# Performance work log

Hardware: AMD Instinct MI355X
Metric: run time of the kernel (lower is better)

Reference implementation:

```python
import jax, jax.numpy as jnp
import numpy as np

DIM = 512
HEADS = 8
DIM_HEAD = 64
CROSS_DIM = 768
FF_INNER = 4 * DIM  # 2048
SCALE = DIM_HEAD ** -0.5
EPS = 1e-5


def _layer_norm(x, g, b):
    mu = jnp.mean(x, axis=-1, keepdims=True)
    var = jnp.var(x, axis=-1, keepdims=True)
    return (x - mu) * jax.lax.rsqrt(var + EPS) * g + b


def _mha(q, k, v):
    # q: [B,Sq,D], k/v: [B,Sk,D] -> [B,Sq,D]
    B, Sq, D = q.shape
    Sk = k.shape[1]
    qh = q.reshape(B, Sq, HEADS, DIM_HEAD).transpose(0, 2, 1, 3)
    kh = k.reshape(B, Sk, HEADS, DIM_HEAD).transpose(0, 2, 1, 3)
    vh = v.reshape(B, Sk, HEADS, DIM_HEAD).transpose(0, 2, 1, 3)
    scores = jnp.einsum('bhqd,bhkd->bhqk', qh, kh) * SCALE
    probs = jax.nn.softmax(scores, axis=-1)
    out = jnp.einsum('bhqk,bhkd->bhqd', probs, vh)
    return out.transpose(0, 2, 1, 3).reshape(B, Sq, D)


def setup_inputs() -> dict:
    key = jax.random.key(0)
    ks = jax.random.split(key, 20)
    s = 0.02
    inp = {
        'x': jax.random.normal(ks[0], (8, 1024, DIM), jnp.float32),
        'enc': jax.random.normal(ks[1], (8, 77, CROSS_DIM), jnp.float32),
        # self-attention (attn1)
        'ln1_g': jnp.ones((DIM,), jnp.float32),
        'ln1_b': jnp.zeros((DIM,), jnp.float32),
        'wq1': jax.random.normal(ks[2], (DIM, DIM), jnp.float32) * s,
        'wk1': jax.random.normal(ks[3], (DIM, DIM), jnp.float32) * s,
        'wv1': jax.random.normal(ks[4], (DIM, DIM), jnp.float32) * s,
        'wo1': jax.random.normal(ks[5], (DIM, DIM), jnp.float32) * s,
        'bo1': jnp.zeros((DIM,), jnp.float32),
        # cross-attention (attn2)
        'ln2_g': jnp.ones((DIM,), jnp.float32),
        'ln2_b': jnp.zeros((DIM,), jnp.float32),
        'wq2': jax.random.normal(ks[6], (DIM, DIM), jnp.float32) * s,
        'wk2': jax.random.normal(ks[7], (CROSS_DIM, DIM), jnp.float32) * s,
        'wv2': jax.random.normal(ks[8], (CROSS_DIM, DIM), jnp.float32) * s,
        'wo2': jax.random.normal(ks[9], (DIM, DIM), jnp.float32) * s,
        'bo2': jnp.zeros((DIM,), jnp.float32),
        # feed-forward (GEGLU)
        'ln3_g': jnp.ones((DIM,), jnp.float32),
        'ln3_b': jnp.zeros((DIM,), jnp.float32),
        'wg': jax.random.normal(ks[10], (DIM, 2 * FF_INNER), jnp.float32) * s,
        'bg': jnp.zeros((2 * FF_INNER,), jnp.float32),
        'wf': jax.random.normal(ks[11], (FF_INNER, DIM), jnp.float32) * s,
        'bf': jnp.zeros((DIM,), jnp.float32),
    }
    return inp


def reference(x, enc, ln1_g, ln1_b, wq1, wk1, wv1, wo1, bo1,
              ln2_g, ln2_b, wq2, wk2, wv2, wo2, bo2,
              ln3_g, ln3_b, wg, bg, wf, bf):
    # self-attention block (pre-norm)
    h = _layer_norm(x, ln1_g, ln1_b)
    a = _mha(h @ wq1, h @ wk1, h @ wv1)
    x = x + a @ wo1 + bo1
    # cross-attention block (pre-norm)
    h = _layer_norm(x, ln2_g, ln2_b)
    a = _mha(h @ wq2, enc @ wk2, enc @ wv2)
    x = x + a @ wo2 + bo2
    # GEGLU feed-forward (pre-norm)
    h = _layer_norm(x, ln3_g, ln3_b)
    proj = h @ wg + bg
    u, g = jnp.split(proj, 2, axis=-1)
    ff = (u * jax.nn.gelu(g, approximate=False)) @ wf + bf
    return x + ff
```

## Files before the change

kernel.cpp:

```cpp
#include <hip/hip_runtime.h>


typedef _Float16 half8 __attribute__((ext_vector_type(8)));
typedef float f32x4 __attribute__((ext_vector_type(4)));

__device__ __forceinline__ f32x4 mfma16(half8 a, half8 b, f32x4 c) {
  return __builtin_amdgcn_mfma_f32_16x16x32_f16(a, b, c, 0, 0, 0);
}

__device__ __forceinline__ void gload16(const _Float16* g, _Float16* l) {
  __builtin_amdgcn_global_load_lds(
      (const __attribute__((address_space(1))) void*)g,
      (__attribute__((address_space(3))) void*)l, 16, 0, 0);
}

__global__ __launch_bounds__(256)
void transpose_cvt(const float* __restrict__ src, _Float16* __restrict__ dst,
                   int K, int N) {
  __shared__ float tile[32][33];
  const int tx = threadIdx.x, ty = threadIdx.y;
  const int n0 = blockIdx.x * 32, k0 = blockIdx.y * 32;
  #pragma unroll
  for (int j = ty; j < 32; j += 8)
    tile[j][tx] = src[(size_t)(k0 + j) * N + n0 + tx];
  __syncthreads();
  #pragma unroll
  for (int j = ty; j < 32; j += 8)
    dst[(size_t)(n0 + j) * K + k0 + tx] = (_Float16)tile[tx][j];
}

__global__ void cvt_f32_f16(const float* __restrict__ src,
                            _Float16* __restrict__ dst, int n) {
  int i = blockIdx.x * 256 + threadIdx.x;
  if (i < n) dst[i] = (_Float16)src[i];
}

__global__ __launch_bounds__(256)
void vt_kernel(const _Float16* __restrict__ src, _Float16* __restrict__ dst,
               int S, int srcStride, int dstStride) {
  __shared__ _Float16 tile[32][33];
  const int tx = threadIdx.x, ty = threadIdx.y;
  const int s0 = blockIdx.x * 32, d0 = blockIdx.y * 32, bh = blockIdx.z;
  const int b = bh >> 3, h = bh & 7;
  const _Float16* sp = src + (size_t)b * S * srcStride + h * 64 + d0;
  #pragma unroll
  for (int j = ty; j < 32; j += 8) {
    int s = s0 + j; if (s >= S) s = S - 1;
    tile[j][tx] = sp[(size_t)s * srcStride + tx];
  }
  __syncthreads();
  _Float16* dp = dst + ((size_t)bh * 64 + d0) * dstStride + s0;
  #pragma unroll
  for (int j = ty; j < 32; j += 8)
    dp[(size_t)j * dstStride + tx] = tile[tx][j];
}

__global__ __launch_bounds__(256)
void ln_kernel(const float* __restrict__ x, const float* __restrict__ g,
               const float* __restrict__ b, _Float16* __restrict__ out) {
  const int row = blockIdx.x, t = threadIdx.x;
  const float* xr = x + (size_t)row * 512;
  float v0 = xr[t], v1 = xr[t + 256];
  float s1 = v0 + v1, s2 = v0 * v0 + v1 * v1;
  #pragma unroll
  for (int m = 32; m >= 1; m >>= 1) {
    s1 += __shfl_xor(s1, m);
    s2 += __shfl_xor(s2, m);
  }
  __shared__ float red[8];
  if ((t & 63) == 0) { red[t >> 6] = s1; red[4 + (t >> 6)] = s2; }
  __syncthreads();
  s1 = red[0] + red[1] + red[2] + red[3];
  s2 = red[4] + red[5] + red[6] + red[7];
  const float mu = s1 * (1.0f / 512.0f);
  const float var = s2 * (1.0f / 512.0f) - mu * mu;
  const float rs = rsqrtf(var + 1e-5f);
  out[(size_t)row * 512 + t] = (_Float16)((v0 - mu) * rs * g[t] + b[t]);
  out[(size_t)row * 512 + t + 256] =
      (_Float16)((v1 - mu) * rs * g[t + 256] + b[t + 256]);
}

template <int EPI, int GWM, int GWN, int WM, int WN, int MW>
__global__ __launch_bounds__(256, MW)
void gemm_bt(const _Float16* __restrict__ A, const _Float16* __restrict__ BT,
             int M, int N, int K, int lda, int ldc,
             _Float16* Ch, float* Cf,
             const float* __restrict__ bias, const float* resid) {
  constexpr int BM = GWM * WM * 16;
  constexpr int BN = GWN * WN * 16;
  __shared__ __align__(16) _Float16 As[2][4 * BM * 8];
  __shared__ __align__(16) _Float16 Bs[2][4 * BN * 8];
  __shared__ __align__(16) _Float16 Bs2[(EPI == 2) ? 2 : 1]
                                      [(EPI == 2) ? 4 * BN * 8 : 8];

  const int t = threadIdx.x;
  const int m0 = blockIdx.y * BM, n0 = blockIdx.x * BN;
  const int lane = t & 63, wv = t >> 6;
  const int quad = lane >> 4, l15 = lane & 15;
  const int wm = wv / GWN, wn = wv % GWN;

  f32x4 zero4 = {0.f, 0.f, 0.f, 0.f};
  f32x4 acc[WM][WN];
  f32x4 acc2[(EPI == 2) ? WM : 1][(EPI == 2) ? WN : 1];
  #pragma unroll
  for (int mi = 0; mi < WM; mi++)
    #pragma unroll
    for (int ni = 0; ni < WN; ni++) acc[mi][ni] = zero4;
  if constexpr (EPI == 2) {
    #pragma unroll
    for (int mi = 0; mi < WM; mi++)
      #pragma unroll
      for (int ni = 0; ni < WN; ni++) acc2[mi][ni] = zero4;
  }

  auto stageAll = [&](int k0, int pb) {
    #pragma unroll
    for (int c = wv; c < BM / 16; c += 4) {
      const int s = c * 64 + lane;
      const int q = s / BM;
      const int r = s % BM;
      int rg = m0 + r; if (rg >= M) rg = M - 1;
      gload16(A + (size_t)rg * lda + k0 + q * 8, &As[pb][c * 512]);
    }
    #pragma unroll
    for (int c = wv; c < BN / 16; c += 4) {
      const int s = c * 64 + lane;
      const int q = s / BN;
      const int r = s % BN;
      gload16(BT + (size_t)(n0 + r) * K + k0 + q * 8, &Bs[pb][c * 512]);
      if constexpr (EPI == 2)
        gload16(BT + (size_t)(2048 + n0 + r) * K + k0 + q * 8,
                &Bs2[pb][c * 512]);
    }
  };

  stageAll(0, 0);
  __syncthreads();

  const int NIT = K >> 5;
  for (int it = 0; it < NIT; ++it) {
    const int cur = it & 1;
    if (it + 1 < NIT) stageAll((it + 1) << 5, cur ^ 1);

    half8 fa[WM], fb[WN], fb2[(EPI == 2) ? WN : 1];
    #pragma unroll
    for (int mi = 0; mi < WM; mi++)
      fa[mi] = *(const half8*)(&As[cur]
          [((size_t)quad * BM + wm * WM * 16 + mi * 16 + l15) * 8]);
    #pragma unroll
    for (int ni = 0; ni < WN; ni++) {
      fb[ni] = *(const half8*)(&Bs[cur]
          [((size_t)quad * BN + wn * WN * 16 + ni * 16 + l15) * 8]);
      if constexpr (EPI == 2)
        fb2[ni] = *(const half8*)(&Bs2[cur]
            [((size_t)quad * BN + wn * WN * 16 + ni * 16 + l15) * 8]);
    }
    #pragma unroll
    for (int mi = 0; mi < WM; mi++)
      #pragma unroll
      for (int ni = 0; ni < WN; ni++) {
        acc[mi][ni] = mfma16(fa[mi], fb[ni], acc[mi][ni]);
        if constexpr (EPI == 2)
          acc2[mi][ni] = mfma16(fa[mi], fb2[ni], acc2[mi][ni]);
      }
    __syncthreads();
  }

  #pragma unroll
  for (int mi = 0; mi < WM; mi++) {
    const int rbase = m0 + wm * WM * 16 + mi * 16 + quad * 4;
    #pragma unroll
    for (int r = 0; r < 4; r++) {
      const int row = rbase + r;
      if (row >= M) continue;
      #pragma unroll
      for (int ni = 0; ni < WN; ni++) {
        const int col = n0 + wn * WN * 16 + ni * 16 + l15;
        const float v = acc[mi][ni][r];
        if constexpr (EPI == 0) {
          Ch[(size_t)row * ldc + col] = (_Float16)v;
        } else if constexpr (EPI == 1) {
          Cf[(size_t)row * ldc + col] =
              resid[(size_t)row * ldc + col] + v + bias[col];
        } else {
          const float u = v + bias[col];
          const float gg = acc2[mi][ni][r] + bias[col + 2048];
          const float ge = 0.5f * gg * (1.0f + erff(gg * 0.70710678118f));
          Ch[(size_t)row * ldc + col] = (_Float16)(u * ge);
        }
      }
    }
  }
}

__global__ __launch_bounds__(256)
void attn2(const _Float16* __restrict__ Q, const _Float16* __restrict__ K,
           const _Float16* __restrict__ VT, _Float16* __restrict__ O,
           int qStride, int kStride, long kBatchStride,
           int vtStride, int Sk) {
  __shared__ __align__(16) _Float16 KsL[2][2048];
  __shared__ __align__(16) _Float16 VTsL[2][2048];
  __shared__ __align__(16) _Float16 Ps[4][2][16][40];

  const int t = threadIdx.x;
  const int w = t >> 6, lane = t & 63, quad = lane >> 4, l15 = lane & 15;
  const int bh = blockIdx.y, b = bh >> 3, h = bh & 7;
  const int q0 = blockIdx.x * 128 + w * 32;

  const _Float16 qscale = (_Float16)(0.125f * 1.44269504f);
  half8 qf[2][2];
  #pragma unroll
  for (int mi = 0; mi < 2; mi++)
    #pragma unroll
    for (int c = 0; c < 2; c++) {
      const _Float16* qp = Q +
          (size_t)(b * 1024 + q0 + mi * 16 + l15) * qStride +
          h * 64 + c * 32 + quad * 8;
      half8 v = *(const half8*)qp;
      #pragma unroll
      for (int j = 0; j < 8; j++) v[j] *= qscale;
      qf[mi][c] = v;
    }

  f32x4 zero4 = {0.f, 0.f, 0.f, 0.f};
  f32x4 oa[2][4];
  float psum[2][4];
  #pragma unroll
  for (int mi = 0; mi < 2; mi++) {
    #pragma unroll
    for (int nt = 0; nt < 4; nt++) oa[mi][nt] = zero4;
    #pragma unroll
    for (int r = 0; r < 4; r++) psum[mi][r] = 0.f;
  }

  const _Float16* kp = K + (size_t)b * kBatchStride + h * 64;
  const _Float16* vtp = VT + (size_t)bh * 64 * vtStride;
  const int ksk = t & 31, kc = t >> 7, kqd = (t >> 5) & 3;
  const int vd = t & 63, vqd = t >> 6;

  auto stageKV = [&](int skb, int pb) {
    int skc = skb + ksk; if (skc >= Sk) skc = Sk - 1;
    gload16(kp + (size_t)skc * kStride + kc * 32 + kqd * 8, &KsL[pb][t * 8]);
    gload16(vtp + (size_t)vd * vtStride + skb + vqd * 8, &VTsL[pb][t * 8]);
  };

  stageKV(0, 0);
  __syncthreads();

  int it = 0;
  for (int skb = 0; skb < Sk; skb += 32, ++it) {
    const int cur = it & 1;
    if (skb + 32 < Sk) stageKV(skb + 32, cur ^ 1);

    const bool tail = (skb + 32 > Sk);
    #pragma unroll
    for (int mi = 0; mi < 2; mi++) {
      #pragma unroll
      for (int ct = 0; ct < 2; ct++) {
        f32x4 s = zero4;
        half8 kb0 = *(const half8*)(&KsL[cur][(quad * 32 + ct * 16 + l15) * 8]);
        half8 kb1 =
            *(const half8*)(&KsL[cur][(128 + quad * 32 + ct * 16 + l15) * 8]);
        s = mfma16(qf[mi][0], kb0, s);
        s = mfma16(qf[mi][1], kb1, s);
        if (tail) {
          const bool valid = (skb + ct * 16 + l15) < Sk;
          #pragma unroll
          for (int r = 0; r < 4; r++)
            if (!valid) s[r] = -__builtin_inff();
        }
        #pragma unroll
        for (int r = 0; r < 4; r++) {
          const float e = exp2f(s[r]);
          psum[mi][r] += e;
          Ps[w][mi][quad * 4 + r][ct * 16 + l15] = (_Float16)e;
        }
      }
    }
    #pragma unroll
    for (int mi = 0; mi < 2; mi++) {
      const half8 pf = *(const half8*)(&Ps[w][mi][l15][quad * 8]);
      #pragma unroll
      for (int nt = 0; nt < 4; nt++) {
        const half8 vf =
            *(const half8*)(&VTsL[cur][(quad * 64 + nt * 16 + l15) * 8]);
        oa[mi][nt] = mfma16(pf, vf, oa[mi][nt]);
      }
    }
    __syncthreads();
  }

  #pragma unroll
  for (int mi = 0; mi < 2; mi++)
    #pragma unroll
    for (int r = 0; r < 4; r++) {
      #pragma unroll
      for (int mm = 1; mm < 16; mm <<= 1)
        psum[mi][r] += __shfl_xor(psum[mi][r], mm);
      psum[mi][r] = 1.0f / psum[mi][r];
    }

  #pragma unroll
  for (int mi = 0; mi < 2; mi++)
    #pragma unroll
    for (int nt = 0; nt < 4; nt++)
      #pragma unroll
      for (int r = 0; r < 4; r++) {
        const size_t row = (size_t)(b * 1024 + q0 + mi * 16 + quad * 4 + r);
        O[row * 512 + h * 64 + nt * 16 + l15] =
            (_Float16)(oa[mi][nt][r] * psum[mi][r]);
      }
}

extern "C" void kernel_launch(void* const* d_in, const int* in_sizes, int n_in,
                              void* d_out, int out_size, void* d_ws,
                              size_t ws_size, hipStream_t stream) {
  const float* x    = (const float*)d_in[0];
  const float* enc  = (const float*)d_in[1];
  const float* ln1g = (const float*)d_in[2];
  const float* ln1b = (const float*)d_in[3];
  const float* wq1  = (const float*)d_in[4];
  const float* wk1  = (const float*)d_in[5];
  const float* wv1  = (const float*)d_in[6];
  const float* wo1  = (const float*)d_in[7];
  const float* bo1  = (const float*)d_in[8];
  const float* ln2g = (const float*)d_in[9];
  const float* ln2b = (const float*)d_in[10];
  const float* wq2  = (const float*)d_in[11];
  const float* wk2  = (const float*)d_in[12];
  const float* wv2  = (const float*)d_in[13];
  const float* wo2  = (const float*)d_in[14];
  const float* bo2  = (const float*)d_in[15];
  const float* ln3g = (const float*)d_in[16];
  const float* ln3b = (const float*)d_in[17];
  const float* wg   = (const float*)d_in[18];
  const float* bg   = (const float*)d_in[19];
  const float* wf   = (const float*)d_in[20];
  const float* bfp  = (const float*)d_in[21];
  float* out = (float*)d_out;

  char* ws = (char*)d_ws;
  _Float16* qkvT  = (_Float16*)(ws + 0);
  _Float16* q2T   = (_Float16*)(ws + 1572864);
  _Float16* kv2T  = (_Float16*)(ws + 2097152);
  _Float16* wo1T  = (_Float16*)(ws + 3670016);
  _Float16* wo2T  = (_Float16*)(ws + 4194304);
  _Float16* wgT   = (_Float16*)(ws + 4718592);
  _Float16* wfT   = (_Float16*)(ws + 8912896);
  _Float16* hbuf  = (_Float16*)(ws + 11010048);
  _Float16* qkv   = (_Float16*)(ws + 19398656);
  _Float16* q2b   = (_Float16*)(ws + 44564480);
  _Float16* kv2b  = (_Float16*)(ws + 52953088);
  _Float16* attnb = (_Float16*)(ws + 54214656);
  _Float16* ench  = (_Float16*)(ws + 62603264);
  _Float16* ffb   = (_Float16*)(ws + 19398656);
  _Float16* VTself = hbuf;
  _Float16* VTc    = ench;

  const dim3 tb(32, 8);
  transpose_cvt<<<dim3(16, 16), tb, 0, stream>>>(wq1, qkvT, 512, 512);
  transpose_cvt<<<dim3(16, 16), tb, 0, stream>>>(wk1, qkvT + 512 * 512, 512, 512);
  transpose_cvt<<<dim3(16, 16), tb, 0, stream>>>(wv1, qkvT + 1024 * 512, 512, 512);
  transpose_cvt<<<dim3(16, 16), tb, 0, stream>>>(wo1, wo1T, 512, 512);
  transpose_cvt<<<dim3(16, 16), tb, 0, stream>>>(wq2, q2T, 512, 512);
  transpose_cvt<<<dim3(16, 24), tb, 0, stream>>>(wk2, kv2T, 768, 512);
  transpose_cvt<<<dim3(16, 24), tb, 0, stream>>>(wv2, kv2T + 512 * 768, 768, 512);
  transpose_cvt<<<dim3(16, 16), tb, 0, stream>>>(wo2, wo2T, 512, 512);
  transpose_cvt<<<dim3(128, 16), tb, 0, stream>>>(wg, wgT, 512, 4096);
  transpose_cvt<<<dim3(16, 64), tb, 0, stream>>>(wf, wfT, 2048, 512);
  cvt_f32_f16<<<(473088 + 255) / 256, 256, 0, stream>>>(enc, ench, 473088);

  ln_kernel<<<8192, 256, 0, stream>>>(x, ln1g, ln1b, hbuf);
  gemm_bt<0, 2, 2, 4, 4, 2><<<dim3(12, 64), 256, 0, stream>>>(
      hbuf, qkvT, 8192, 1536, 512, 512, 1536, qkv, nullptr, nullptr, nullptr);
  vt_kernel<<<dim3(32, 2, 64), tb, 0, stream>>>(qkv + 1024, VTself, 1024, 1536, 1024);
  attn2<<<dim3(8, 64), 256, 0, stream>>>(qkv, qkv + 512, VTself, attnb,
                                         1536, 1536, (long)1024 * 1536,
                                         1024, 1024);
  gemm_bt<1, 1, 4, 4, 2, 3><<<dim3(4, 128), 256, 0, stream>>>(
      attnb, wo1T, 8192, 512, 512, 512, 512, nullptr, out, bo1, x);

  ln_kernel<<<8192, 256, 0, stream>>>(out, ln2g, ln2b, hbuf);
  gemm_bt<0, 1, 4, 4, 2, 3><<<dim3(4, 128), 256, 0, stream>>>(
      hbuf, q2T, 8192, 512, 512, 512, 512, q2b, nullptr, nullptr, nullptr);
  gemm_bt<0, 1, 4, 4, 2, 3><<<dim3(8, 10), 256, 0, stream>>>(
      ench, kv2T, 616, 1024, 768, 768, 1024, kv2b, nullptr, nullptr, nullptr);
  vt_kernel<<<dim3(3, 2, 64), tb, 0, stream>>>(kv2b + 512, VTc, 77, 1024, 96);
  attn2<<<dim3(8, 64), 256, 0, stream>>>(q2b, kv2b, VTc, attnb,
                                         512, 1024, (long)77 * 1024, 96, 77);
  gemm_bt<1, 1, 4, 4, 2, 3><<<dim3(4, 128), 256, 0, stream>>>(
      attnb, wo2T, 8192, 512, 512, 512, 512, nullptr, out, bo2, out);

  ln_kernel<<<8192, 256, 0, stream>>>(out, ln3g, ln3b, hbuf);
  gemm_bt<2, 2, 2, 4, 2, 2><<<dim3(32, 64), 256, 0, stream>>>(
      hbuf, wgT, 8192, 2048, 512, 512, 2048, ffb, nullptr, bg, nullptr);
  gemm_bt<1, 1, 4, 4, 2, 3><<<dim3(4, 128), 256, 0, stream>>>(
      ffb, wfT, 8192, 512, 2048, 2048, 512, nullptr, out, bfp, out);
}
```

Measured before the change: 495.0 us.

## Merge weight prep launches and add XCD-aware block swizzle to GEMMs

```diff
diff --git a/kernel.cpp b/kernel.cpp
--- a/kernel.cpp
+++ b/kernel.cpp
@@ -14,12 +14,36 @@
       (__attribute__((address_space(3))) void*)l, 16, 0, 0);
 }
 
+struct PrepArgs {
+  const float* src[10];
+  _Float16* dst[10];
+  int K[10], N[10], base[10];
+  const float* enc;
+  _Float16* ench;
+  int encBase, nEnc;
+};
+
 __global__ __launch_bounds__(256)
-void transpose_cvt(const float* __restrict__ src, _Float16* __restrict__ dst,
-                   int K, int N) {
+void prep_all(PrepArgs pa) {
   __shared__ float tile[32][33];
+  const int bid = blockIdx.x;
   const int tx = threadIdx.x, ty = threadIdx.y;
-  const int n0 = blockIdx.x * 32, k0 = blockIdx.y * 32;
+  if (bid >= pa.encBase) {
+    const int i = (bid - pa.encBase) * 256 + ty * 32 + tx;
+    if (i < pa.nEnc) pa.ench[i] = (_Float16)pa.enc[i];
+    return;
+  }
+  int mi = 0;
+  #pragma unroll
+  for (int j = 1; j < 10; j++)
+    if (bid >= pa.base[j]) mi = j;
+  const int K = pa.K[mi], N = pa.N[mi];
+  const int rel = bid - pa.base[mi];
+  const int ntiles = N >> 5;
+  const int bx = rel % ntiles, by = rel / ntiles;
+  const float* src = pa.src[mi];
+  _Float16* dst = pa.dst[mi];
+  const int n0 = bx * 32, k0 = by * 32;
   #pragma unroll
   for (int j = ty; j < 32; j += 8)
     tile[j][tx] = src[(size_t)(k0 + j) * N + n0 + tx];
@@ -27,12 +51,6 @@
   #pragma unroll
   for (int j = ty; j < 32; j += 8)
     dst[(size_t)(n0 + j) * K + k0 + tx] = (_Float16)tile[tx][j];
-}
-
-__global__ void cvt_f32_f16(const float* __restrict__ src,
-                            _Float16* __restrict__ dst, int n) {
-  int i = blockIdx.x * 256 + threadIdx.x;
-  if (i < n) dst[i] = (_Float16)src[i];
 }
 
 __global__ __launch_bounds__(256)
@@ -80,7 +98,7 @@
       (_Float16)((v1 - mu) * rs * g[t + 256] + b[t + 256]);
 }
 
-template <int EPI, int GWM, int GWN, int WM, int WN, int MW>
+template <int EPI, int GWM, int GWN, int WM, int WN, int MW, int SWZ>
 __global__ __launch_bounds__(256, MW)
 void gemm_bt(const _Float16* __restrict__ A, const _Float16* __restrict__ BT,
              int M, int N, int K, int lda, int ldc,
@@ -94,7 +112,19 @@
                                       [(EPI == 2) ? 4 * BN * 8 : 8];
 
   const int t = threadIdx.x;
-  const int m0 = blockIdx.y * BM, n0 = blockIdx.x * BN;
+  const int NNB = (N + BN - 1) / BN;
+  int bm, bn;
+  if constexpr (SWZ) {
+    const int MG = (M / BM) >> 3;
+    const int xcd = blockIdx.x & 7;
+    const int s = blockIdx.x >> 3;
+    bm = xcd * MG + s % MG;
+    bn = s / MG;
+  } else {
+    bn = blockIdx.x % NNB;
+    bm = blockIdx.x / NNB;
+  }
+  const int m0 = bm * BM, n0 = bn * BN;
   const int lane = t & 63, wv = t >> 6;
   const int quad = lane >> 4, l15 = lane & 15;
   const int wm = wv / GWN, wn = wv % GWN;
@@ -357,43 +387,48 @@
   _Float16* VTself = hbuf;
   _Float16* VTc    = ench;
 
+  PrepArgs pa;
+  const float* srcs[10] = {wq1, wk1, wv1, wo1, wq2, wk2, wv2, wo2, wg, wf};
+  _Float16* dsts[10] = {qkvT, qkvT + 512 * 512, qkvT + 1024 * 512, wo1T, q2T,
+                        kv2T, kv2T + 512 * 768, wo2T, wgT, wfT};
+  const int Ks[10] = {512, 512, 512, 512, 512, 768, 768, 512, 512, 2048};
+  const int Ns[10] = {512, 512, 512, 512, 512, 512, 512, 512, 4096, 512};
+  int base = 0;
+  for (int i = 0; i < 10; i++) {
+    pa.src[i] = srcs[i]; pa.dst[i] = dsts[i];
+    pa.K[i] = Ks[i]; pa.N[i] = Ns[i]; pa.base[i] = base;
+    base += (Ks[i] >> 5) * (Ns[i] >> 5);
+  }
+  pa.enc = enc; pa.ench = ench; pa.encBase = base; pa.nEnc = 473088;
+  const int prepBlocks = base + (473088 + 255) / 256;
+  prep_all<<<prepBlocks, dim3(32, 8), 0, stream>>>(pa);
+
   const dim3 tb(32, 8);
-  transpose_cvt<<<dim3(16, 16), tb, 0, stream>>>(wq1, qkvT, 512, 512);
-  transpose_cvt<<<dim3(16, 16), tb, 0, stream>>>(wk1, qkvT + 512 * 512, 512, 512);
-  transpose_cvt<<<dim3(16, 16), tb, 0, stream>>>(wv1, qkvT + 1024 * 512, 512, 512);
-  transpose_cvt<<<dim3(16, 16), tb, 0, stream>>>(wo1, wo1T, 512, 512);
-  transpose_cvt<<<dim3(16, 16), tb, 0, stream>>>(wq2, q2T, 512, 512);
-  transpose_cvt<<<dim3(16, 24), tb, 0, stream>>>(wk2, kv2T, 768, 512);
-  transpose_cvt<<<dim3(16, 24), tb, 0, stream>>>(wv2, kv2T + 512 * 768, 768, 512);
-  transpose_cvt<<<dim3(16, 16), tb, 0, stream>>>(wo2, wo2T, 512, 512);
-  transpose_cvt<<<dim3(128, 16), tb, 0, stream>>>(wg, wgT, 512, 4096);
-  transpose_cvt<<<dim3(16, 64), tb, 0, stream>>>(wf, wfT, 2048, 512);
-  cvt_f32_f16<<<(473088 + 255) / 256, 256, 0, stream>>>(enc, ench, 473088);
 
   ln_kernel<<<8192, 256, 0, stream>>>(x, ln1g, ln1b, hbuf);
-  gemm_bt<0, 2, 2, 4, 4, 2><<<dim3(12, 64), 256, 0, stream>>>(
+  gemm_bt<0, 2, 2, 4, 4, 2, 1><<<768, 256, 0, stream>>>(
       hbuf, qkvT, 8192, 1536, 512, 512, 1536, qkv, nullptr, nullptr, nullptr);
   vt_kernel<<<dim3(32, 2, 64), tb, 0, stream>>>(qkv + 1024, VTself, 1024, 1536, 1024);
   attn2<<<dim3(8, 64), 256, 0, stream>>>(qkv, qkv + 512, VTself, attnb,
                                          1536, 1536, (long)1024 * 1536,
                                          1024, 1024);
-  gemm_bt<1, 1, 4, 4, 2, 3><<<dim3(4, 128), 256, 0, stream>>>(
+  gemm_bt<1, 1, 4, 4, 2, 3, 1><<<512, 256, 0, stream>>>(
       attnb, wo1T, 8192, 512, 512, 512, 512, nullptr, out, bo1, x);
 
   ln_kernel<<<8192, 256, 0, stream>>>(out, ln2g, ln2b, hbuf);
-  gemm_bt<0, 1, 4, 4, 2, 3><<<dim3(4, 128), 256, 0, stream>>>(
+  gemm_bt<0, 1, 4, 4, 2, 3, 1><<<512, 256, 0, stream>>>(
       hbuf, q2T, 8192, 512, 512, 512, 512, q2b, nullptr, nullptr, nullptr);
-  gemm_bt<0, 1, 4, 4, 2, 3><<<dim3(8, 10), 256, 0, stream>>>(
+  gemm_bt<0, 1, 4, 4, 2, 3, 0><<<80, 256, 0, stream>>>(
       ench, kv2T, 616, 1024, 768, 768, 1024, kv2b, nullptr, nullptr, nullptr);
   vt_kernel<<<dim3(3, 2, 64), tb, 0, stream>>>(kv2b + 512, VTc, 77, 1024, 96);
   attn2<<<dim3(8, 64), 256, 0, stream>>>(q2b, kv2b, VTc, attnb,
                                          512, 1024, (long)77 * 1024, 96, 77);
-  gemm_bt<1, 1, 4, 4, 2, 3><<<dim3(4, 128), 256, 0, stream>>>(
+  gemm_bt<1, 1, 4, 4, 2, 3, 1><<<512, 256, 0, stream>>>(
       attnb, wo2T, 8192, 512, 512, 512, 512, nullptr, out, bo2, out);
 
   ln_kernel<<<8192, 256, 0, stream>>>(out, ln3g, ln3b, hbuf);
-  gemm_bt<2, 2, 2, 4, 2, 2><<<dim3(32, 64), 256, 0, stream>>>(
+  gemm_bt<2, 2, 2, 4, 2, 2, 1><<<2048, 256, 0, stream>>>(
       hbuf, wgT, 8192, 2048, 512, 512, 2048, ffb, nullptr, bg, nullptr);
-  gemm_bt<1, 1, 4, 4, 2, 3><<<dim3(4, 128), 256, 0, stream>>>(
+  gemm_bt<1, 1, 4, 4, 2, 3, 1><<<512, 256, 0, stream>>>(
       ffb, wfT, 8192, 512, 2048, 2048, 512, nullptr, out, bfp, out);
 }
```

Result: faster. 460.9 us (-6.9%).
